# Optimization experiments

Measured on AMD Instinct MI355X. Metric: run time of the kernel, lower is better.

The kernel has to match this reference:

```python
import jax, jax.numpy as jnp
import numpy as np

B, S, D = 4, 2048, 1024
E = 8           # num_experts
TOP_K = 2
H = 3 * D       # hidden_mult = 3


def setup_inputs() -> dict:
    key = jax.random.key(0)
    ks = jax.random.split(key, 5)
    scale_d = 1.0 / np.sqrt(D)
    scale_h = 1.0 / np.sqrt(H)
    return {
        "x": jax.random.normal(ks[0], (B, S, D), dtype=jnp.float32),
        "gate_w": jax.random.normal(ks[1], (D, E), dtype=jnp.float32) * scale_d,
        "w1": jax.random.normal(ks[2], (E, D, H), dtype=jnp.float32) * scale_d,
        "w3": jax.random.normal(ks[3], (E, D, H), dtype=jnp.float32) * scale_d,
        "w2": jax.random.normal(ks[4], (E, H, D), dtype=jnp.float32) * scale_h,
    }


def reference(x, gate_w, w1, w2, w3):
    b, s, d = x.shape
    t = b * s
    xf = x.reshape(t, d)                                  # [T, D]
    probs = jax.nn.softmax(xf @ gate_w, axis=-1)          # [T, E]
    vals, idx = jax.lax.top_k(probs, TOP_K)               # [T, K]
    w = vals / jnp.sum(vals, axis=-1, keepdims=True)      # renormalized top-k weights
    # per-token combine weight for each expert (scatter top-k weights)
    comb = jnp.zeros((t, E), dtype=x.dtype).at[
        jnp.arange(t)[:, None], idx
    ].add(w)                                              # [T, E]
    out = jnp.zeros_like(xf)
    for e in range(E):  # small fixed expert count
        h = jax.nn.silu(xf @ w1[e]) * (xf @ w3[e])        # [T, H] SwiGLU
        out = out + comb[:, e:e + 1] * (h @ w2[e])        # weighted combine
    return out.reshape(b, s, d)
```

## Files before the change

kernel.cpp:

```cpp
#include <hip/hip_runtime.h>
#include <stdint.h>

#define T_TOK 8192
#define DDIM 1024
#define NEXP 8
#define HDIM 3072

typedef __attribute__((ext_vector_type(8))) short bfrag;
typedef __attribute__((ext_vector_type(4))) float facc;

__device__ __forceinline__ void gload16(const void* g, void* l) {
  __builtin_amdgcn_global_load_lds(
      (const __attribute__((address_space(1))) void*)g,
      (__attribute__((address_space(3))) void*)l, 16, 0, 0);
}

__device__ __forceinline__ unsigned short f2bf(float f) {
  unsigned int u = __float_as_uint(f);
  u += 0x7FFFu + ((u >> 16) & 1u);
  return (unsigned short)(u >> 16);
}

__global__ __launch_bounds__(64) void gate_topk(
    const float* __restrict__ x, const float* __restrict__ gw,
    int* __restrict__ counts, int* __restrict__ tok_list,
    float* __restrict__ wt_list, int* __restrict__ slotA,
    int* __restrict__ slotB)
{
  const int t = blockIdx.x;
  const int lane = threadIdx.x;
  const float* xr = x + (size_t)t * DDIM;
  float p[NEXP];
#pragma unroll
  for (int e = 0; e < NEXP; ++e) p[e] = 0.f;
#pragma unroll 4
  for (int i = 0; i < DDIM / 64; ++i) {
    const int d = i * 64 + lane;
    const float xv = xr[d];
    const float4 g0 = *(const float4*)(gw + (size_t)d * NEXP);
    const float4 g1 = *(const float4*)(gw + (size_t)d * NEXP + 4);
    p[0] += xv * g0.x; p[1] += xv * g0.y; p[2] += xv * g0.z; p[3] += xv * g0.w;
    p[4] += xv * g1.x; p[5] += xv * g1.y; p[6] += xv * g1.z; p[7] += xv * g1.w;
  }
#pragma unroll
  for (int off = 32; off > 0; off >>= 1) {
#pragma unroll
    for (int e = 0; e < NEXP; ++e) p[e] += __shfl_down(p[e], off);
  }
  if (lane == 0) {
    int i1 = 0; float v1 = p[0];
#pragma unroll
    for (int e = 1; e < NEXP; ++e) if (p[e] > v1) { v1 = p[e]; i1 = e; }
    int i2 = -1; float v2 = -3.4e38f;
#pragma unroll
    for (int e = 0; e < NEXP; ++e) if (e != i1 && p[e] > v2) { v2 = p[e]; i2 = e; }
    const float w0 = 1.f / (1.f + __expf(v2 - v1));
    int q1 = atomicAdd(&counts[i1 * 32], 1);
    tok_list[i1 * T_TOK + q1] = t;
    wt_list[i1 * T_TOK + q1] = w0;
    slotA[t] = i1 * T_TOK + q1;
    int q2 = atomicAdd(&counts[i2 * 32], 1);
    tok_list[i2 * T_TOK + q2] = t;
    wt_list[i2 * T_TOK + q2] = 1.f - w0;
    slotB[t] = i2 * T_TOK + q2;
  }
}

__global__ void calc_offs(const int* __restrict__ counts, int* __restrict__ offs) {
  if (threadIdx.x == 0 && blockIdx.x == 0) {
    int a = 0;
#pragma unroll
    for (int e = 0; e < NEXP; ++e) { offs[e] = a; a += counts[e * 32]; }
    offs[NEXP] = a;
  }
}

__global__ __launch_bounds__(256) void convert_x(
    const float* __restrict__ x, unsigned short* __restrict__ xb)
{
  const size_t i8 = ((size_t)blockIdx.x * 256 + threadIdx.x) * 8;
  const float4 a = *(const float4*)(x + i8);
  const float4 b = *(const float4*)(x + i8 + 4);
  union { unsigned short s[8]; uint4 v; } t;
  t.s[0] = f2bf(a.x); t.s[1] = f2bf(a.y); t.s[2] = f2bf(a.z); t.s[3] = f2bf(a.w);
  t.s[4] = f2bf(b.x); t.s[5] = f2bf(b.y); t.s[6] = f2bf(b.z); t.s[7] = f2bf(b.w);
  *(uint4*)(xb + i8) = t.v;
}

__global__ __launch_bounds__(256) void convert_wT(
    const float* __restrict__ src, unsigned short* __restrict__ dst,
    int K, int N)
{
  const int e = blockIdx.z;
  const int k0 = blockIdx.x * 64;
  const int n0 = blockIdx.y * 128;
  const float* se = src + (size_t)e * K * N;
  unsigned short* de = dst + (size_t)e * N * K;
  __shared__ unsigned short Tb[64][130];
  const int tid = threadIdx.x;
#pragma unroll
  for (int i = 0; i < 8; ++i) {
    const int f = i * 256 + tid;
    const int kl = f >> 5, nq = (f & 31) * 4;
    const float4 v = *(const float4*)(se + (size_t)(k0 + kl) * N + n0 + nq);
    Tb[kl][nq + 0] = f2bf(v.x);
    Tb[kl][nq + 1] = f2bf(v.y);
    Tb[kl][nq + 2] = f2bf(v.z);
    Tb[kl][nq + 3] = f2bf(v.w);
  }
  __syncthreads();
#pragma unroll
  for (int i = 0; i < 4; ++i) {
    const int idx = i * 256 + tid;
    const int n = idx >> 3, up = idx & 7;
    const int kb = (up ^ (n & 7)) * 8;
    union { unsigned short s[8]; uint4 v; } t;
#pragma unroll
    for (int j = 0; j < 8; ++j) t.s[j] = Tb[kb + j][n];
    *(uint4*)(de + ((size_t)(n0 + n) * K + k0 + up * 8)) = t.v;
  }
}

__global__ __launch_bounds__(256, 2) void moe_gemm1(
    const unsigned short* __restrict__ xb, const unsigned short* __restrict__ w1t,
    const unsigned short* __restrict__ w3t, const int* __restrict__ counts,
    const int* __restrict__ offs, const int* __restrict__ tok_list,
    unsigned short* __restrict__ h_buf)
{
  const int e = blockIdx.z;
  const int cnt = counts[e * 32];
  const int p0 = blockIdx.y * 128;
  if (p0 >= cnt) return;
  const int n0 = blockIdx.x * 128;
  const int hbase = offs[e];

  __shared__ __align__(16) unsigned short lds[24576];
  unsigned short* As  = lds;
  unsigned short* B1s = lds + 8192;
  unsigned short* B3s = lds + 16384;

  const int tid = threadIdx.x;
  const int lane = tid & 63;
  const int wv = tid >> 6;
  const int wm = wv >> 1;
  const int wn = wv & 1;
  const int lr = lane & 15;
  const int lg = lane >> 4;
  const int l8 = lane >> 3;
  const int lu = lane & 7;
  const int aswz = (lu ^ l8) * 16;

  const int* tl = tok_list + e * T_TOK;

  const unsigned short* asrc[4];
#pragma unroll
  for (int i = 0; i < 4; ++i) {
    const int p = p0 + wv * 32 + i * 8 + l8;
    const int tok = (p < cnt) ? tl[p] : 0;
    asrc[i] = xb + (size_t)tok * DDIM;
  }
  const unsigned short* b1src[4];
  const unsigned short* b3src[4];
#pragma unroll
  for (int i = 0; i < 4; ++i) {
    const int n = n0 + wv * 32 + i * 8 + l8;
    b1src[i] = w1t + (size_t)(e * HDIM + n) * DDIM;
    b3src[i] = w3t + (size_t)(e * HDIM + n) * DDIM;
  }

  facc acc1[4][4], acc3[4][4];
#pragma unroll
  for (int m = 0; m < 4; ++m)
#pragma unroll
    for (int n = 0; n < 4; ++n)
#pragma unroll
      for (int q = 0; q < 4; ++q) { acc1[m][n][q] = 0.f; acc3[m][n][q] = 0.f; }

#pragma unroll 1
  for (int k0 = 0; k0 < DDIM; k0 += 64) {
#pragma unroll
    for (int i = 0; i < 4; ++i)
      gload16((const char*)asrc[i] + k0 * 2 + aswz, &As[(wv * 4 + i) * 512]);
#pragma unroll
    for (int i = 0; i < 4; ++i)
      gload16((const char*)b1src[i] + k0 * 2 + lu * 16, &B1s[(wv * 4 + i) * 512]);
#pragma unroll
    for (int i = 0; i < 4; ++i)
      gload16((const char*)b3src[i] + k0 * 2 + lu * 16, &B3s[(wv * 4 + i) * 512]);
    __syncthreads();
#pragma unroll
    for (int ks = 0; ks < 2; ++ks) {
      bfrag a[4];
#pragma unroll
      for (int m = 0; m < 4; ++m) {
        const int r = wm * 64 + m * 16 + lr;
        const int u = (ks * 4 + lg) ^ (r & 7);
        a[m] = *(const bfrag*)&As[r * 64 + u * 8];
      }
#pragma unroll
      for (int n = 0; n < 4; ++n) {
        const int rb = wn * 64 + n * 16 + lr;
        const int u = (ks * 4 + lg) ^ (rb & 7);
        const bfrag b1 = *(const bfrag*)&B1s[rb * 64 + u * 8];
#pragma unroll
        for (int m = 0; m < 4; ++m)
          acc1[m][n] = __builtin_amdgcn_mfma_f32_16x16x32_bf16(a[m], b1, acc1[m][n], 0, 0, 0);
        const bfrag b3 = *(const bfrag*)&B3s[rb * 64 + u * 8];
#pragma unroll
        for (int m = 0; m < 4; ++m)
          acc3[m][n] = __builtin_amdgcn_mfma_f32_16x16x32_bf16(a[m], b3, acc3[m][n], 0, 0, 0);
      }
    }
    __syncthreads();
  }

#pragma unroll
  for (int m = 0; m < 4; ++m)
#pragma unroll
    for (int n = 0; n < 4; ++n)
#pragma unroll
      for (int q = 0; q < 4; ++q) {
        const float a1 = acc1[m][n][q];
        const float a3 = acc3[m][n][q];
        const float hv = a1 * a3 / (1.f + __expf(-a1));
        const int row = wm * 64 + m * 16 + lg * 4 + q;
        const int col = wn * 64 + n * 16 + lr;
        lds[row * 128 + col] = f2bf(hv);
      }
  __syncthreads();
#pragma unroll
  for (int i = 0; i < 8; ++i) {
    const int idx = i * 256 + tid;
    const int r = idx >> 4, u = idx & 15;
    if (p0 + r < cnt)
      *(uint4*)(h_buf + ((size_t)(hbase + p0 + r) * HDIM + n0 + u * 8)) =
          *(const uint4*)&lds[r * 128 + u * 8];
  }
}

__global__ __launch_bounds__(256, 2) void moe_gemm2(
    const unsigned short* __restrict__ h_buf, const unsigned short* __restrict__ w2t,
    const int* __restrict__ counts, const int* __restrict__ offs,
    float* __restrict__ part)
{
  const int e = blockIdx.z;
  const int cnt = counts[e * 32];
  const int p0 = blockIdx.y * 128;
  if (p0 >= cnt) return;
  const int n0 = blockIdx.x * 128;
  const int hbase = offs[e];

  __shared__ __align__(16) unsigned short Ah[128 * 64];
  __shared__ __align__(16) unsigned short Bw[128 * 64];

  const int tid = threadIdx.x;
  const int lane = tid & 63;
  const int wv = tid >> 6;
  const int wm = wv >> 1;
  const int wn = wv & 1;
  const int lr = lane & 15;
  const int lg = lane >> 4;
  const int l8 = lane >> 3;
  const int lu = lane & 7;
  const int aswz = (lu ^ l8) * 16;

  const unsigned short* asrc[4];
#pragma unroll
  for (int i = 0; i < 4; ++i) {
    const int p = p0 + wv * 32 + i * 8 + l8;
    const int hrow = hbase + ((p < cnt) ? p : 0);
    asrc[i] = h_buf + (size_t)hrow * HDIM;
  }
  const unsigned short* bsrc[4];
#pragma unroll
  for (int i = 0; i < 4; ++i) {
    const int n = n0 + wv * 32 + i * 8 + l8;
    bsrc[i] = w2t + (size_t)(e * DDIM + n) * HDIM;
  }

  facc acc[4][4];
#pragma unroll
  for (int m = 0; m < 4; ++m)
#pragma unroll
    for (int n = 0; n < 4; ++n)
#pragma unroll
      for (int q = 0; q < 4; ++q) acc[m][n][q] = 0.f;

#pragma unroll 1
  for (int k0 = 0; k0 < HDIM; k0 += 64) {
#pragma unroll
    for (int i = 0; i < 4; ++i)
      gload16((const char*)asrc[i] + k0 * 2 + aswz, &Ah[(wv * 4 + i) * 512]);
#pragma unroll
    for (int i = 0; i < 4; ++i)
      gload16((const char*)bsrc[i] + k0 * 2 + lu * 16, &Bw[(wv * 4 + i) * 512]);
    __syncthreads();
#pragma unroll
    for (int ks = 0; ks < 2; ++ks) {
      bfrag a[4];
#pragma unroll
      for (int m = 0; m < 4; ++m) {
        const int r = wm * 64 + m * 16 + lr;
        const int u = (ks * 4 + lg) ^ (r & 7);
        a[m] = *(const bfrag*)&Ah[r * 64 + u * 8];
      }
#pragma unroll
      for (int n = 0; n < 4; ++n) {
        const int rb = wn * 64 + n * 16 + lr;
        const int u = (ks * 4 + lg) ^ (rb & 7);
        const bfrag b = *(const bfrag*)&Bw[rb * 64 + u * 8];
#pragma unroll
        for (int m = 0; m < 4; ++m)
          acc[m][n] = __builtin_amdgcn_mfma_f32_16x16x32_bf16(a[m], b, acc[m][n], 0, 0, 0);
      }
    }
    __syncthreads();
  }

#pragma unroll
  for (int m = 0; m < 4; ++m)
#pragma unroll
    for (int q = 0; q < 4; ++q) {
      const int p = p0 + wm * 64 + m * 16 + lg * 4 + q;
      if (p < cnt) {
        float* dst = part + (size_t)(hbase + p) * DDIM + n0 + wn * 64 + lr;
#pragma unroll
        for (int n = 0; n < 4; ++n)
          dst[n * 16] = acc[m][n][q];
      }
    }
}

__global__ __launch_bounds__(256) void combine_out(
    const float* __restrict__ part, const int* __restrict__ slotA,
    const int* __restrict__ slotB, const float* __restrict__ wt_list,
    const int* __restrict__ offs, float* __restrict__ out)
{
  const int t = blockIdx.x;
  const int sA = slotA[t], sB = slotB[t];
  const float wA = wt_list[sA], wB = wt_list[sB];
  const int pA = offs[sA >> 13] + (sA & (T_TOK - 1));
  const int pB = offs[sB >> 13] + (sB & (T_TOK - 1));
  const float* ra = part + (size_t)pA * DDIM;
  const float* rb = part + (size_t)pB * DDIM;
  float* o = out + (size_t)t * DDIM;
  const int i = threadIdx.x * 4;
  const float4 a = *(const float4*)(ra + i);
  const float4 b = *(const float4*)(rb + i);
  float4 r;
  r.x = wA * a.x + wB * b.x;
  r.y = wA * a.y + wB * b.y;
  r.z = wA * a.z + wB * b.z;
  r.w = wA * a.w + wB * b.w;
  *(float4*)(o + i) = r;
}

__global__ __launch_bounds__(64) void gate_topk_fb(
    const float* __restrict__ x, const float* __restrict__ gw,
    int* __restrict__ counts, int* __restrict__ tok_list,
    float* __restrict__ wt_list)
{
  const int t = blockIdx.x;
  const int lane = threadIdx.x;
  const float* xr = x + (size_t)t * DDIM;
  float p[NEXP];
#pragma unroll
  for (int e = 0; e < NEXP; ++e) p[e] = 0.f;
#pragma unroll 4
  for (int i = 0; i < DDIM / 64; ++i) {
    const int d = i * 64 + lane;
    const float xv = xr[d];
    const float4 g0 = *(const float4*)(gw + (size_t)d * NEXP);
    const float4 g1 = *(const float4*)(gw + (size_t)d * NEXP + 4);
    p[0] += xv * g0.x; p[1] += xv * g0.y; p[2] += xv * g0.z; p[3] += xv * g0.w;
    p[4] += xv * g1.x; p[5] += xv * g1.y; p[6] += xv * g1.z; p[7] += xv * g1.w;
  }
#pragma unroll
  for (int off = 32; off > 0; off >>= 1) {
#pragma unroll
    for (int e = 0; e < NEXP; ++e) p[e] += __shfl_down(p[e], off);
  }
  if (lane == 0) {
    int i1 = 0; float v1 = p[0];
#pragma unroll
    for (int e = 1; e < NEXP; ++e) if (p[e] > v1) { v1 = p[e]; i1 = e; }
    int i2 = -1; float v2 = -3.4e38f;
#pragma unroll
    for (int e = 0; e < NEXP; ++e) if (e != i1 && p[e] > v2) { v2 = p[e]; i2 = e; }
    const float w0 = 1.f / (1.f + __expf(v2 - v1));
    int q1 = atomicAdd(&counts[i1 * 32], 1);
    tok_list[i1 * T_TOK + q1] = t;
    wt_list[i1 * T_TOK + q1] = w0;
    int q2 = atomicAdd(&counts[i2 * 32], 1);
    tok_list[i2 * T_TOK + q2] = t;
    wt_list[i2 * T_TOK + q2] = 1.f - w0;
  }
}

__global__ __launch_bounds__(256) void moe_gemm1_fb(
    const float* __restrict__ x, const float* __restrict__ w1,
    const float* __restrict__ w3, const int* __restrict__ counts,
    const int* __restrict__ tok_list, unsigned short* __restrict__ h_buf,
    int e)
{
  const int cnt = counts[e * 32];
  const int p0 = blockIdx.y * 64;
  if (p0 >= cnt) return;
  const int n0 = blockIdx.x * 64;

  __shared__ unsigned short As[64][40];
  __shared__ unsigned short B1s[64][40];
  __shared__ unsigned short B3s[64][40];

  const int tid = threadIdx.x;
  const int lane = tid & 63;
  const int wv = tid >> 6;

  const float* w1e = w1 + (size_t)e * DDIM * HDIM;
  const float* w3e = w3 + (size_t)e * DDIM * HDIM;
  const int* tl = tok_list + e * T_TOK;

  const int arow = tid >> 2;
  const int akseg = (tid & 3) * 8;
  int tok = -1;
  if (p0 + arow < cnt) tok = tl[p0 + arow];

  const int bk = tid >> 3;
  const int bn4 = (tid & 7) * 4;

  facc acc1[4], acc3[4];
#pragma unroll
  for (int i = 0; i < 4; ++i)
#pragma unroll
    for (int j = 0; j < 4; ++j) { acc1[i][j] = 0.f; acc3[i][j] = 0.f; }

  const int mrow = wv * 16 + (lane & 15);
  const int kq = (lane >> 4) * 8;

  for (int k0 = 0; k0 < DDIM; k0 += 32) {
    {
      union { unsigned short s[8]; uint4 v; } tmp;
      if (tok >= 0) {
        const float* src = x + (size_t)tok * DDIM + k0 + akseg;
        const float4 f0 = *(const float4*)(src);
        const float4 f1 = *(const float4*)(src + 4);
        tmp.s[0]=f2bf(f0.x); tmp.s[1]=f2bf(f0.y); tmp.s[2]=f2bf(f0.z); tmp.s[3]=f2bf(f0.w);
        tmp.s[4]=f2bf(f1.x); tmp.s[5]=f2bf(f1.y); tmp.s[6]=f2bf(f1.z); tmp.s[7]=f2bf(f1.w);
      } else {
        tmp.v = make_uint4(0u, 0u, 0u, 0u);
      }
      *(uint4*)&As[arow][akseg] = tmp.v;
    }
#pragma unroll
    for (int pass = 0; pass < 2; ++pass) {
      const int n = bn4 + pass * 32;
      const float4 f1v = *(const float4*)(w1e + (size_t)(k0 + bk) * HDIM + n0 + n);
      B1s[n + 0][bk] = f2bf(f1v.x);
      B1s[n + 1][bk] = f2bf(f1v.y);
      B1s[n + 2][bk] = f2bf(f1v.z);
      B1s[n + 3][bk] = f2bf(f1v.w);
      const float4 f3v = *(const float4*)(w3e + (size_t)(k0 + bk) * HDIM + n0 + n);
      B3s[n + 0][bk] = f2bf(f3v.x);
      B3s[n + 1][bk] = f2bf(f3v.y);
      B3s[n + 2][bk] = f2bf(f3v.z);
      B3s[n + 3][bk] = f2bf(f3v.w);
    }
    __syncthreads();
    const bfrag a = *(const bfrag*)&As[mrow][kq];
#pragma unroll
    for (int nt = 0; nt < 4; ++nt) {
      const bfrag b1 = *(const bfrag*)&B1s[nt * 16 + (lane & 15)][kq];
      acc1[nt] = __builtin_amdgcn_mfma_f32_16x16x32_bf16(a, b1, acc1[nt], 0, 0, 0);
      const bfrag b3 = *(const bfrag*)&B3s[nt * 16 + (lane & 15)][kq];
      acc3[nt] = __builtin_amdgcn_mfma_f32_16x16x32_bf16(a, b3, acc3[nt], 0, 0, 0);
    }
    __syncthreads();
  }
  const int rbase = p0 + wv * 16 + ((lane >> 4) * 4);
  const int cbase = n0 + (lane & 15);
#pragma unroll
  for (int r = 0; r < 4; ++r) {
    const int p = rbase + r;
    if (p < cnt) {
      unsigned short* dst = h_buf + (size_t)p * HDIM + cbase;
#pragma unroll
      for (int nt = 0; nt < 4; ++nt) {
        const float a1 = acc1[nt][r];
        const float a3 = acc3[nt][r];
        const float hv = a1 * a3 / (1.f + __expf(-a1));
        dst[nt * 16] = f2bf(hv);
      }
    }
  }
}

__global__ __launch_bounds__(256) void moe_gemm2_fb(
    const unsigned short* __restrict__ h_buf, const float* __restrict__ w2,
    const int* __restrict__ counts, const int* __restrict__ tok_list,
    const float* __restrict__ wt_list, float* __restrict__ out, int e)
{
  const int cnt = counts[e * 32];
  const int p0 = blockIdx.y * 64;
  if (p0 >= cnt) return;
  const int n0 = blockIdx.x * 64;

  __shared__ unsigned short As[64][40];
  __shared__ unsigned short Bs[64][40];

  const int tid = threadIdx.x;
  const int lane = tid & 63;
  const int wv = tid >> 6;

  const float* w2e = w2 + (size_t)e * HDIM * DDIM;
  const int* tl = tok_list + e * T_TOK;
  const float* wl = wt_list + e * T_TOK;

  const int arow = tid >> 2;
  const int akseg = (tid & 3) * 8;
  const bool avalid = (p0 + arow < cnt);

  const int bk = tid >> 3;
  const int bn4 = (tid & 7) * 4;

  facc acc[4];
#pragma unroll
  for (int i = 0; i < 4; ++i)
#pragma unroll
    for (int j = 0; j < 4; ++j) acc[i][j] = 0.f;

  const int mrow = wv * 16 + (lane & 15);
  const int kq = (lane >> 4) * 8;

  for (int k0 = 0; k0 < HDIM; k0 += 32) {
    if (avalid) {
      *(uint4*)&As[arow][akseg] =
          *(const uint4*)(h_buf + (size_t)(p0 + arow) * HDIM + k0 + akseg);
    } else {
      *(uint4*)&As[arow][akseg] = make_uint4(0u, 0u, 0u, 0u);
    }
#pragma unroll
    for (int pass = 0; pass < 2; ++pass) {
      const int n = bn4 + pass * 32;
      const float4 f = *(const float4*)(w2e + (size_t)(k0 + bk) * DDIM + n0 + n);
      Bs[n + 0][bk] = f2bf(f.x);
      Bs[n + 1][bk] = f2bf(f.y);
      Bs[n + 2][bk] = f2bf(f.z);
      Bs[n + 3][bk] = f2bf(f.w);
    }
    __syncthreads();
    const bfrag a = *(const bfrag*)&As[mrow][kq];
#pragma unroll
    for (int nt = 0; nt < 4; ++nt) {
      const bfrag b = *(const bfrag*)&Bs[nt * 16 + (lane & 15)][kq];
      acc[nt] = __builtin_amdgcn_mfma_f32_16x16x32_bf16(a, b, acc[nt], 0, 0, 0);
    }
    __syncthreads();
  }
  const int rbase = p0 + wv * 16 + ((lane >> 4) * 4);
  const int cbase = n0 + (lane & 15);
#pragma unroll
  for (int r = 0; r < 4; ++r) {
    const int p = rbase + r;
    if (p < cnt) {
      const int tok = tl[p];
      const float wt = wl[p];
      float* dst = out + (size_t)tok * DDIM + cbase;
#pragma unroll
      for (int nt = 0; nt < 4; ++nt) {
        atomicAdd(dst + nt * 16, acc[nt][r] * wt);
      }
    }
  }
}

__global__ void ws_too_small(float* out, int n) {
  int i = blockIdx.x * 256 + threadIdx.x;
  if (i < n) out[i] = 1.0e6f;
}

extern "C" void kernel_launch(void* const* d_in, const int* in_sizes, int n_in,
                              void* d_out, int out_size, void* d_ws, size_t ws_size,
                              hipStream_t stream) {
  const float* x  = (const float*)d_in[0];
  const float* gw = (const float*)d_in[1];
  const float* w1 = (const float*)d_in[2];
  const float* w3 = (const float*)d_in[3];
  const float* w2 = (const float*)d_in[4];
  float* out = (float*)d_out;

  const size_t off_tok = 4096;
  const size_t off_wt  = off_tok + (size_t)NEXP * T_TOK * 4;
  const size_t off_sA  = off_wt + (size_t)NEXP * T_TOK * 4;
  const size_t off_sB  = off_sA + (size_t)T_TOK * 4;
  const size_t off_xb  = off_sB + (size_t)T_TOK * 4;
  const size_t off_w1t = off_xb + (size_t)T_TOK * DDIM * 2;
  const size_t off_w3t = off_w1t + (size_t)NEXP * DDIM * HDIM * 2;
  const size_t off_w2t = off_w3t + (size_t)NEXP * DDIM * HDIM * 2;
  const size_t off_h   = off_w2t + (size_t)NEXP * HDIM * DDIM * 2;
  const size_t need    = off_h + (size_t)(2 * T_TOK) * HDIM * 2;
  const size_t off_part = off_w1t;

  if (ws_size >= need) {
    int* counts = (int*)d_ws;
    int* offs = (int*)((char*)d_ws + 1024);
    int* tok_list = (int*)((char*)d_ws + off_tok);
    float* wt_list = (float*)((char*)d_ws + off_wt);
    int* slotA = (int*)((char*)d_ws + off_sA);
    int* slotB = (int*)((char*)d_ws + off_sB);
    unsigned short* xb  = (unsigned short*)((char*)d_ws + off_xb);
    unsigned short* w1t = (unsigned short*)((char*)d_ws + off_w1t);
    unsigned short* w3t = (unsigned short*)((char*)d_ws + off_w3t);
    unsigned short* w2t = (unsigned short*)((char*)d_ws + off_w2t);
    unsigned short* h_buf = (unsigned short*)((char*)d_ws + off_h);
    float* part = (float*)((char*)d_ws + off_part);

    hipMemsetAsync(d_ws, 0, 4096, stream);

    convert_x<<<(T_TOK * DDIM) / (256 * 8), 256, 0, stream>>>(x, xb);
    convert_wT<<<dim3(DDIM / 64, HDIM / 128, NEXP), 256, 0, stream>>>(w1, w1t, DDIM, HDIM);
    convert_wT<<<dim3(DDIM / 64, HDIM / 128, NEXP), 256, 0, stream>>>(w3, w3t, DDIM, HDIM);
    convert_wT<<<dim3(HDIM / 64, DDIM / 128, NEXP), 256, 0, stream>>>(w2, w2t, HDIM, DDIM);
    gate_topk<<<T_TOK, 64, 0, stream>>>(x, gw, counts, tok_list, wt_list, slotA, slotB);
    calc_offs<<<1, 1, 0, stream>>>(counts, offs);
    moe_gemm1<<<dim3(HDIM / 128, T_TOK / 128, NEXP), 256, 0, stream>>>(
        xb, w1t, w3t, counts, offs, tok_list, h_buf);
    moe_gemm2<<<dim3(DDIM / 128, T_TOK / 128, NEXP), 256, 0, stream>>>(
        h_buf, w2t, counts, offs, part);
    combine_out<<<T_TOK, 256, 0, stream>>>(part, slotA, slotB, wt_list, offs, out);
    return;
  }

  const size_t fb_off_tok = 1024;
  const size_t fb_off_wt  = fb_off_tok + (size_t)NEXP * T_TOK * 4;
  const size_t fb_off_h   = fb_off_wt + (size_t)NEXP * T_TOK * 4;
  const size_t fb_need    = fb_off_h + (size_t)T_TOK * HDIM * 2;
  if (ws_size < fb_need) {
    ws_too_small<<<(out_size + 255) / 256, 256, 0, stream>>>(out, out_size);
    return;
  }
  int* counts = (int*)d_ws;
  int* tok_list = (int*)((char*)d_ws + fb_off_tok);
  float* wt_list = (float*)((char*)d_ws + fb_off_wt);
  unsigned short* h_buf = (unsigned short*)((char*)d_ws + fb_off_h);

  hipMemsetAsync(counts, 0, 1024, stream);
  hipMemsetAsync(out, 0, (size_t)out_size * sizeof(float), stream);

  gate_topk_fb<<<T_TOK, 64, 0, stream>>>(x, gw, counts, tok_list, wt_list);
  for (int e = 0; e < NEXP; ++e) {
    moe_gemm1_fb<<<dim3(HDIM / 64, T_TOK / 64), 256, 0, stream>>>(
        x, w1, w3, counts, tok_list, h_buf, e);
    moe_gemm2_fb<<<dim3(DDIM / 64, T_TOK / 64), 256, 0, stream>>>(
        h_buf, w2, counts, tok_list, wt_list, out, e);
  }
}
```

Measured before the change: 765.3 us.

## Fuse x conversion into gating, merge w1/w3 conversion, halve gemm1 N tile

The x-to-bf16 conversion moves into the gate_topk kernel, which already reads x, so one launch and one pass over x are removed. The w1 and w3 transposed conversions are merged into a single launch. moe_gemm1 drops its N tile from 128 to 64, which halves its accumulators and LDS use. That should allow more resident waves and more blocks, at the cost of re-reading the A tile more often and lower MFMA reuse per loaded A fragment.

```diff
diff --git a/kernel.cpp b/kernel.cpp
--- a/kernel.cpp
+++ b/kernel.cpp
@@ -25,11 +25,12 @@
     const float* __restrict__ x, const float* __restrict__ gw,
     int* __restrict__ counts, int* __restrict__ tok_list,
     float* __restrict__ wt_list, int* __restrict__ slotA,
-    int* __restrict__ slotB)
+    int* __restrict__ slotB, unsigned short* __restrict__ xb)
 {
   const int t = blockIdx.x;
   const int lane = threadIdx.x;
   const float* xr = x + (size_t)t * DDIM;
+  unsigned short* xbr = xb + (size_t)t * DDIM;
   float p[NEXP];
 #pragma unroll
   for (int e = 0; e < NEXP; ++e) p[e] = 0.f;
@@ -37,6 +38,7 @@
   for (int i = 0; i < DDIM / 64; ++i) {
     const int d = i * 64 + lane;
     const float xv = xr[d];
+    xbr[d] = f2bf(xv);
     const float4 g0 = *(const float4*)(gw + (size_t)d * NEXP);
     const float4 g1 = *(const float4*)(gw + (size_t)d * NEXP + 4);
     p[0] += xv * g0.x; p[1] += xv * g0.y; p[2] += xv * g0.z; p[3] += xv * g0.w;
@@ -75,27 +77,10 @@
   }
 }
 
-__global__ __launch_bounds__(256) void convert_x(
-    const float* __restrict__ x, unsigned short* __restrict__ xb)
-{
-  const size_t i8 = ((size_t)blockIdx.x * 256 + threadIdx.x) * 8;
-  const float4 a = *(const float4*)(x + i8);
-  const float4 b = *(const float4*)(x + i8 + 4);
-  union { unsigned short s[8]; uint4 v; } t;
-  t.s[0] = f2bf(a.x); t.s[1] = f2bf(a.y); t.s[2] = f2bf(a.z); t.s[3] = f2bf(a.w);
-  t.s[4] = f2bf(b.x); t.s[5] = f2bf(b.y); t.s[6] = f2bf(b.z); t.s[7] = f2bf(b.w);
-  *(uint4*)(xb + i8) = t.v;
-}
-
-__global__ __launch_bounds__(256) void convert_wT(
-    const float* __restrict__ src, unsigned short* __restrict__ dst,
-    int K, int N)
-{
-  const int e = blockIdx.z;
-  const int k0 = blockIdx.x * 64;
-  const int n0 = blockIdx.y * 128;
-  const float* se = src + (size_t)e * K * N;
-  unsigned short* de = dst + (size_t)e * N * K;
+__device__ __forceinline__ void conv_tile(
+    const float* __restrict__ se, unsigned short* __restrict__ de,
+    int K, int N, int k0, int n0)
+{
   __shared__ unsigned short Tb[64][130];
   const int tid = threadIdx.x;
 #pragma unroll
@@ -121,6 +106,25 @@
   }
 }
 
+__global__ __launch_bounds__(256) void convert_w13(
+    const float* __restrict__ w1, const float* __restrict__ w3,
+    unsigned short* __restrict__ w1t, unsigned short* __restrict__ w3t)
+{
+  const int zz = blockIdx.z;
+  const int e = zz & (NEXP - 1);
+  const float* se = (zz < NEXP ? w1 : w3) + (size_t)e * DDIM * HDIM;
+  unsigned short* de = (zz < NEXP ? w1t : w3t) + (size_t)e * HDIM * DDIM;
+  conv_tile(se, de, DDIM, HDIM, blockIdx.x * 64, blockIdx.y * 128);
+}
+
+__global__ __launch_bounds__(256) void convert_w2(
+    const float* __restrict__ w2, unsigned short* __restrict__ w2t)
+{
+  const int e = blockIdx.z;
+  conv_tile(w2 + (size_t)e * HDIM * DDIM, w2t + (size_t)e * DDIM * HDIM,
+            HDIM, DDIM, blockIdx.x * 64, blockIdx.y * 128);
+}
+
 __global__ __launch_bounds__(256, 2) void moe_gemm1(
     const unsigned short* __restrict__ xb, const unsigned short* __restrict__ w1t,
     const unsigned short* __restrict__ w3t, const int* __restrict__ counts,
@@ -131,13 +135,12 @@
   const int cnt = counts[e * 32];
   const int p0 = blockIdx.y * 128;
   if (p0 >= cnt) return;
-  const int n0 = blockIdx.x * 128;
+  const int n0 = blockIdx.x * 64;
   const int hbase = offs[e];
 
-  __shared__ __align__(16) unsigned short lds[24576];
-  unsigned short* As  = lds;
-  unsigned short* B1s = lds + 8192;
-  unsigned short* B3s = lds + 16384;
+  __shared__ __align__(16) unsigned short As[128 * 64];
+  __shared__ __align__(16) unsigned short B1s[64 * 64];
+  __shared__ __align__(16) unsigned short B3s[64 * 64];
 
   const int tid = threadIdx.x;
   const int lane = tid & 63;
@@ -159,20 +162,20 @@
     const int tok = (p < cnt) ? tl[p] : 0;
     asrc[i] = xb + (size_t)tok * DDIM;
   }
-  const unsigned short* b1src[4];
-  const unsigned short* b3src[4];
-#pragma unroll
-  for (int i = 0; i < 4; ++i) {
-    const int n = n0 + wv * 32 + i * 8 + l8;
+  const unsigned short* b1src[2];
+  const unsigned short* b3src[2];
+#pragma unroll
+  for (int i = 0; i < 2; ++i) {
+    const int n = n0 + wv * 16 + i * 8 + l8;
     b1src[i] = w1t + (size_t)(e * HDIM + n) * DDIM;
     b3src[i] = w3t + (size_t)(e * HDIM + n) * DDIM;
   }
 
-  facc acc1[4][4], acc3[4][4];
+  facc acc1[4][2], acc3[4][2];
 #pragma unroll
   for (int m = 0; m < 4; ++m)
 #pragma unroll
-    for (int n = 0; n < 4; ++n)
+    for (int n = 0; n < 2; ++n)
 #pragma unroll
       for (int q = 0; q < 4; ++q) { acc1[m][n][q] = 0.f; acc3[m][n][q] = 0.f; }
 
@@ -182,11 +185,10 @@
     for (int i = 0; i < 4; ++i)
       gload16((const char*)asrc[i] + k0 * 2 + aswz, &As[(wv * 4 + i) * 512]);
 #pragma unroll
-    for (int i = 0; i < 4; ++i)
-      gload16((const char*)b1src[i] + k0 * 2 + lu * 16, &B1s[(wv * 4 + i) * 512]);
-#pragma unroll
-    for (int i = 0; i < 4; ++i)
-      gload16((const char*)b3src[i] + k0 * 2 + lu * 16, &B3s[(wv * 4 + i) * 512]);
+    for (int i = 0; i < 2; ++i) {
+      gload16((const char*)b1src[i] + k0 * 2 + lu * 16, &B1s[(wv * 2 + i) * 512]);
+      gload16((const char*)b3src[i] + k0 * 2 + lu * 16, &B3s[(wv * 2 + i) * 512]);
+    }
     __syncthreads();
 #pragma unroll
     for (int ks = 0; ks < 2; ++ks) {
@@ -198,8 +200,8 @@
         a[m] = *(const bfrag*)&As[r * 64 + u * 8];
       }
 #pragma unroll
-      for (int n = 0; n < 4; ++n) {
-        const int rb = wn * 64 + n * 16 + lr;
+      for (int n = 0; n < 2; ++n) {
+        const int rb = wn * 32 + n * 16 + lr;
         const int u = (ks * 4 + lg) ^ (rb & 7);
         const bfrag b1 = *(const bfrag*)&B1s[rb * 64 + u * 8];
 #pragma unroll
@@ -217,24 +219,24 @@
 #pragma unroll
   for (int m = 0; m < 4; ++m)
 #pragma unroll
-    for (int n = 0; n < 4; ++n)
+    for (int n = 0; n < 2; ++n)
 #pragma unroll
       for (int q = 0; q < 4; ++q) {
         const float a1 = acc1[m][n][q];
         const float a3 = acc3[m][n][q];
         const float hv = a1 * a3 / (1.f + __expf(-a1));
         const int row = wm * 64 + m * 16 + lg * 4 + q;
-        const int col = wn * 64 + n * 16 + lr;
-        lds[row * 128 + col] = f2bf(hv);
+        const int col = wn * 32 + n * 16 + lr;
+        As[row * 64 + col] = f2bf(hv);
       }
   __syncthreads();
 #pragma unroll
-  for (int i = 0; i < 8; ++i) {
+  for (int i = 0; i < 4; ++i) {
     const int idx = i * 256 + tid;
-    const int r = idx >> 4, u = idx & 15;
+    const int r = idx >> 3, u = idx & 7;
     if (p0 + r < cnt)
       *(uint4*)(h_buf + ((size_t)(hbase + p0 + r) * HDIM + n0 + u * 8)) =
-          *(const uint4*)&lds[r * 128 + u * 8];
+          *(const uint4*)&As[r * 64 + u * 8];
   }
 }
 
@@ -616,13 +618,13 @@
 
     hipMemsetAsync(d_ws, 0, 4096, stream);
 
-    convert_x<<<(T_TOK * DDIM) / (256 * 8), 256, 0, stream>>>(x, xb);
-    convert_wT<<<dim3(DDIM / 64, HDIM / 128, NEXP), 256, 0, stream>>>(w1, w1t, DDIM, HDIM);
-    convert_wT<<<dim3(DDIM / 64, HDIM / 128, NEXP), 256, 0, stream>>>(w3, w3t, DDIM, HDIM);
-    convert_wT<<<dim3(HDIM / 64, DDIM / 128, NEXP), 256, 0, stream>>>(w2, w2t, HDIM, DDIM);
-    gate_topk<<<T_TOK, 64, 0, stream>>>(x, gw, counts, tok_list, wt_list, slotA, slotB);
+    convert_w13<<<dim3(DDIM / 64, HDIM / 128, 2 * NEXP), 256, 0, stream>>>(
+        w1, w3, w1t, w3t);
+    convert_w2<<<dim3(HDIM / 64, DDIM / 128, NEXP), 256, 0, stream>>>(w2, w2t);
+    gate_topk<<<T_TOK, 64, 0, stream>>>(x, gw, counts, tok_list, wt_list,
+                                        slotA, slotB, xb);
     calc_offs<<<1, 1, 0, stream>>>(counts, offs);
-    moe_gemm1<<<dim3(HDIM / 128, T_TOK / 128, NEXP), 256, 0, stream>>>(
+    moe_gemm1<<<dim3(HDIM / 64, T_TOK / 128, NEXP), 256, 0, stream>>>(
         xb, w1t, w3t, counts, offs, tok_list, h_buf);
     moe_gemm2<<<dim3(DDIM / 128, T_TOK / 128, NEXP), 256, 0, stream>>>(
         h_buf, w2t, counts, offs, part);
```

New measurement: 736.4 us. 1.04x faster.
